# Kernel tuning notes

Measured on AMD Instinct MI355X. Metric: run time of the kernel, lower is better.

The kernel has to match this reference:

```python
import jax, jax.numpy as jnp
import numpy as np

B, H, A, D = 4096, 50, 32, 64          # batch, history len, neighbor count, embed_dim
NU, NV = 100000, 100000                # num users, num items
L = H + A                              # total gathered entries per node


def setup_inputs() -> dict:
    key = jax.random.key(0)
    ks = jax.random.split(key, 16)
    # embedding tables (u2e/v2e uniform(-1,1) as in module init, r2e ~ N(0,1) default)
    u2e = jax.random.uniform(ks[0], (NU, D), minval=-1.0, maxval=1.0, dtype=jnp.float32)
    v2e = jax.random.uniform(ks[1], (NV, D), minval=-1.0, maxval=1.0, dtype=jnp.float32)
    r2e = jax.random.normal(ks[2], (7, D), dtype=jnp.float32)
    relation_att = jax.random.normal(ks[3], (2 * D,), dtype=jnp.float32)
    s = 1.0 / np.sqrt(2 * D)  # torch Linear default init bound
    agg_W = jax.random.uniform(ks[4], (D, 2 * D), minval=-s, maxval=s, dtype=jnp.float32)
    agg_b = jax.random.uniform(ks[5], (D,), minval=-s, maxval=s, dtype=jnp.float32)
    lin1_W = jax.random.uniform(ks[6], (D, 2 * D), minval=-s, maxval=s, dtype=jnp.float32)
    lin1_b = jax.random.uniform(ks[7], (D,), minval=-s, maxval=s, dtype=jnp.float32)
    nodes_u = jax.random.randint(ks[8], (B,), 0, NU)
    nodes_v = jax.random.randint(ks[9], (B,), 0, NV)
    hist_u = jax.random.randint(ks[10], (B, H), 0, NV)   # user history = items
    hist_ur = jax.random.randint(ks[11], (B, H), 0, 6)   # ratings 0..5
    adj_u = jax.random.randint(ks[12], (B, A), 0, NU)    # social neighbors = users
    hist_v = jax.random.randint(ks[13], (B, H), 0, NU)   # item history = users
    hist_vr = jax.random.randint(ks[14], (B, H), 0, 6)
    adj_v = jax.random.randint(ks[15], (B, A), 0, NV)    # item-adj neighbors = items
    return dict(u2e=u2e, v2e=v2e, r2e=r2e, relation_att=relation_att,
                agg_W=agg_W, agg_b=agg_b, lin1_W=lin1_W, lin1_b=lin1_b,
                nodes_u=nodes_u, nodes_v=nodes_v,
                hist_u=hist_u, hist_ur=hist_ur, adj_u=adj_u,
                hist_v=hist_v, hist_vr=hist_vr, adj_v=adj_v)


def _encode(node_tab, target_tab, hist_tab, neigh_tab, r2e, relation_att,
            agg_W, agg_b, lin1_W, lin1_b, nodes, targets, hn, hr, adj):
    # Node_Encoder.forward + Node_Aggregator (percent=1.0 -> deterministic:
    # multinomial selects all indices; softmax-weighted sum is permutation-invariant).
    nf = node_tab[nodes]                                   # [B, D]
    tf = target_tab[targets]                               # [B, D]
    # query (computed as in original; with percent=1 the norm-softmax sampling
    # probability does not affect the output)
    _q = jnp.concatenate([nf, tf], axis=-1) @ agg_W.T + agg_b  # [B, D]
    hist_feat = jnp.concatenate([hist_tab[hn], neigh_tab[adj]], axis=1)  # [B, L, D]
    rates = jnp.concatenate([hr, jnp.full(adj.shape, 6, dtype=hr.dtype)], axis=1)
    rate_feat = r2e[rates]                                 # [B, L, D]
    sel = jnp.concatenate([hist_feat, rate_feat], axis=-1)  # [B, L, 2D]
    logits = jnp.einsum('ble,e->bl', sel, relation_att)    # [B, L]
    p = jax.nn.softmax(logits, axis=1)                     # softmax2 over entries
    neigh = jnp.einsum('bl,bld->bd', p, hist_feat)         # weighted sum [B, D]
    comb = jnp.concatenate([nf, neigh], axis=-1)           # [B, 2D]
    return jax.nn.relu(comb @ lin1_W.T + lin1_b)           # [B, D]


def reference(u2e, v2e, r2e, relation_att, agg_W, agg_b, lin1_W, lin1_b,
              nodes_u, nodes_v, hist_u, hist_ur, adj_u, hist_v, hist_vr, adj_v):
    # user side: isitem=False -> node=u2e, target=v2e, hist=v2e, neighbor=u2e
    eu = _encode(u2e, v2e, v2e, u2e, r2e, relation_att, agg_W, agg_b, lin1_W, lin1_b,
                 nodes_u, nodes_v, hist_u, hist_ur, adj_u)
    # item side: isitem=True -> node=v2e, target=u2e, hist=u2e, neighbor=v2e
    ev = _encode(v2e, u2e, u2e, v2e, r2e, relation_att, agg_W, agg_b, lin1_W, lin1_b,
                 nodes_v, nodes_u, hist_v, hist_vr, adj_v)
    return jnp.sum(eu * ev, axis=1)                        # [B]
```

## Files before the change

kernel.cpp:

```cpp
#include <hip/hip_runtime.h>


#define NB 4096
#define NH 50
#define NA 32
#define ND 64

__global__ void rlog_setup(const float* __restrict__ r2e,
                           const float* __restrict__ ra,
                           float* __restrict__ ws_rlog)
{
    const int lane = threadIdx.x;
    const float ra_hi = ra[64 + lane];
    #pragma unroll
    for (int r = 0; r < 7; ++r) {
        float part = r2e[r * 64 + lane] * ra_hi;
        #pragma unroll
        for (int off = 32; off >= 1; off >>= 1)
            part += __shfl_xor(part, off);
        if (lane == 0) ws_rlog[r] = part;
    }
}

__global__ __launch_bounds__(256, 8) void graphconsis_main(
    const float* __restrict__ u2e, const float* __restrict__ v2e,
    const float* __restrict__ ra,
    const float* __restrict__ lin1_W, const float* __restrict__ lin1_b,
    const int* __restrict__ nodes_u, const int* __restrict__ nodes_v,
    const int* __restrict__ hist_u, const int* __restrict__ hist_ur,
    const int* __restrict__ adj_u,
    const int* __restrict__ hist_v, const int* __restrict__ hist_vr,
    const int* __restrict__ adj_v,
    const float* __restrict__ ws_rlog,
    float* __restrict__ out)
{
    __shared__ float lds_comb[4][128];
    __shared__ float ed[4][64];

    const int wid  = threadIdx.x >> 6;
    const int lane = threadIdx.x & 63;
    const int g    = lane >> 4;
    const int j    = lane & 15;
    const int side = wid >> 1;
    const int b    = __builtin_amdgcn_readfirstlane(blockIdx.x * 2 + (wid & 1));

    const float* nodeTab  = side ? v2e : u2e;
    const float* histTab  = side ? u2e : v2e;
    const float* neighTab = side ? v2e : u2e;
    const int* nodes = side ? nodes_v : nodes_u;
    const int* hn    = side ? hist_v  : hist_u;
    const int* hr    = side ? hist_vr : hist_ur;
    const int* adj   = side ? adj_v   : adj_u;

    const float4 ra4  = *(const float4*)(ra + 4 * j);
    const float rlog6 = ws_rlog[6];

    int hidx[13];
    #pragma unroll
    for (int k = 0; k < 13; ++k) {
        int l = 4 * k + g; if (l > NH - 1) l = NH - 1;
        hidx[k] = hn[b * NH + l];
    }
    float rl0 = 0.f;
    { int l = 4 * j + g; if (l < NH) rl0 = ws_rlog[hr[b * NH + l]]; }

    float ssum = 0.f;
    float4 acc = make_float4(0.f, 0.f, 0.f, 0.f);

    #pragma unroll 4
    for (int k = 0; k < 12; ++k) {
        const float4 e = *(const float4*)(histTab + hidx[k] * ND + 4 * j);
        float part = e.x * ra4.x;
        part = fmaf(e.y, ra4.y, part);
        part = fmaf(e.z, ra4.z, part);
        part = fmaf(e.w, ra4.w, part);
        part += (j == k) ? rl0 : 0.f;
        part += __shfl_xor(part, 1);
        part += __shfl_xor(part, 2);
        part += __shfl_xor(part, 4);
        part += __shfl_xor(part, 8);
        const float p = __expf(part);
        ssum += p;
        acc.x = fmaf(p, e.x, acc.x);
        acc.y = fmaf(p, e.y, acc.y);
        acc.z = fmaf(p, e.z, acc.z);
        acc.w = fmaf(p, e.w, acc.w);
    }
    {
        const float4 e = *(const float4*)(histTab + hidx[12] * ND + 4 * j);
        float part = e.x * ra4.x;
        part = fmaf(e.y, ra4.y, part);
        part = fmaf(e.z, ra4.z, part);
        part = fmaf(e.w, ra4.w, part);
        part += (j == 12) ? rl0 : 0.f;
        part += __shfl_xor(part, 1);
        part += __shfl_xor(part, 2);
        part += __shfl_xor(part, 4);
        part += __shfl_xor(part, 8);
        const float p = (g < 2) ? __expf(part) : 0.f;
        ssum += p;
        acc.x = fmaf(p, e.x, acc.x);
        acc.y = fmaf(p, e.y, acc.y);
        acc.z = fmaf(p, e.z, acc.z);
        acc.w = fmaf(p, e.w, acc.w);
    }
    #pragma unroll 4
    for (int k = 0; k < 8; ++k) {
        const int idx = adj[b * NA + 4 * k + g];
        const float4 e = *(const float4*)(neighTab + idx * ND + 4 * j);
        float part = e.x * ra4.x;
        part = fmaf(e.y, ra4.y, part);
        part = fmaf(e.z, ra4.z, part);
        part = fmaf(e.w, ra4.w, part);
        part += __shfl_xor(part, 1);
        part += __shfl_xor(part, 2);
        part += __shfl_xor(part, 4);
        part += __shfl_xor(part, 8);
        const float p = __expf(part + rlog6);
        ssum += p;
        acc.x = fmaf(p, e.x, acc.x);
        acc.y = fmaf(p, e.y, acc.y);
        acc.z = fmaf(p, e.z, acc.z);
        acc.w = fmaf(p, e.w, acc.w);
    }

    ssum += __shfl_xor(ssum, 16);
    ssum += __shfl_xor(ssum, 32);
    acc.x += __shfl_xor(acc.x, 16); acc.x += __shfl_xor(acc.x, 32);
    acc.y += __shfl_xor(acc.y, 16); acc.y += __shfl_xor(acc.y, 32);
    acc.z += __shfl_xor(acc.z, 16); acc.z += __shfl_xor(acc.z, 32);
    acc.w += __shfl_xor(acc.w, 16); acc.w += __shfl_xor(acc.w, 32);

    const float inv = 1.0f / ssum;
    const float4 nf4 = *(const float4*)(nodeTab + nodes[b] * ND + 4 * j);

    if (g == 0) {
        *(float4*)&lds_comb[wid][4 * j] = nf4;
        float4 n4 = make_float4(acc.x * inv, acc.y * inv, acc.z * inv, acc.w * inv);
        *(float4*)&lds_comb[wid][64 + 4 * j] = n4;
    }

    float o = lin1_b[lane];
    const float4* W4 = (const float4*)(lin1_W + lane * 128);
    const float4* C4 = (const float4*)lds_comb[wid];
    #pragma unroll 8
    for (int kk = 0; kk < 32; ++kk) {
        const float4 w = W4[kk];
        const float4 c = C4[kk];
        o = fmaf(w.x, c.x, o);
        o = fmaf(w.y, c.y, o);
        o = fmaf(w.z, c.z, o);
        o = fmaf(w.w, c.w, o);
    }
    const float evec = fmaxf(o, 0.f);

    ed[wid][lane] = evec;
    __syncthreads();

    if (wid < 2) {
        float prod = ed[wid][lane] * ed[wid + 2][lane];
        #pragma unroll
        for (int off = 32; off >= 1; off >>= 1)
            prod += __shfl_xor(prod, off);
        if (lane == 0) out[blockIdx.x * 2 + wid] = prod;
    }
}

extern "C" void kernel_launch(void* const* d_in, const int* in_sizes, int n_in,
                              void* d_out, int out_size, void* d_ws, size_t ws_size,
                              hipStream_t stream)
{
    const float* u2e     = (const float*)d_in[0];
    const float* v2e     = (const float*)d_in[1];
    const float* r2e     = (const float*)d_in[2];
    const float* ra      = (const float*)d_in[3];
    const float* lin1_W  = (const float*)d_in[6];
    const float* lin1_b  = (const float*)d_in[7];
    const int* nodes_u   = (const int*)d_in[8];
    const int* nodes_v   = (const int*)d_in[9];
    const int* hist_u    = (const int*)d_in[10];
    const int* hist_ur   = (const int*)d_in[11];
    const int* adj_u     = (const int*)d_in[12];
    const int* hist_v    = (const int*)d_in[13];
    const int* hist_vr   = (const int*)d_in[14];
    const int* adj_v     = (const int*)d_in[15];
    float* out = (float*)d_out;
    float* ws_rlog = (float*)d_ws;

    hipLaunchKernelGGL(rlog_setup, dim3(1), dim3(64), 0, stream, r2e, ra, ws_rlog);
    hipLaunchKernelGGL(graphconsis_main, dim3(NB / 2), dim3(256), 0, stream,
                       u2e, v2e, ra, lin1_W, lin1_b,
                       nodes_u, nodes_v, hist_u, hist_ur, adj_u,
                       hist_v, hist_vr, adj_v, ws_rlog, out);
}
```

Before: 59.13 us.

## Fuse rating-logit setup into main kernel and prefetch all gathered rows upfront

Removes the separate single-block rlog_setup launch. Each block now computes the seven rating logits in wave 0, stores them in LDS and synchronises before use. All 21 embedding-row gathers plus the node row are issued into registers before any compute, to expose more memory-level parallelism. The launch-bounds occupancy hint is dropped, and the register arrays raise VGPR pressure, which may reduce occupancy.

```diff
diff --git a/kernel.cpp b/kernel.cpp
--- a/kernel.cpp
+++ b/kernel.cpp
@@ -6,34 +6,18 @@
 #define NA 32
 #define ND 64
 
-__global__ void rlog_setup(const float* __restrict__ r2e,
-                           const float* __restrict__ ra,
-                           float* __restrict__ ws_rlog)
-{
-    const int lane = threadIdx.x;
-    const float ra_hi = ra[64 + lane];
-    #pragma unroll
-    for (int r = 0; r < 7; ++r) {
-        float part = r2e[r * 64 + lane] * ra_hi;
-        #pragma unroll
-        for (int off = 32; off >= 1; off >>= 1)
-            part += __shfl_xor(part, off);
-        if (lane == 0) ws_rlog[r] = part;
-    }
-}
-
-__global__ __launch_bounds__(256, 8) void graphconsis_main(
+__global__ __launch_bounds__(256) void graphconsis_main(
     const float* __restrict__ u2e, const float* __restrict__ v2e,
-    const float* __restrict__ ra,
+    const float* __restrict__ r2e, const float* __restrict__ ra,
     const float* __restrict__ lin1_W, const float* __restrict__ lin1_b,
     const int* __restrict__ nodes_u, const int* __restrict__ nodes_v,
     const int* __restrict__ hist_u, const int* __restrict__ hist_ur,
     const int* __restrict__ adj_u,
     const int* __restrict__ hist_v, const int* __restrict__ hist_vr,
     const int* __restrict__ adj_v,
-    const float* __restrict__ ws_rlog,
     float* __restrict__ out)
 {
+    __shared__ float rlog_lds[8];
     __shared__ float lds_comb[4][128];
     __shared__ float ed[4][64];
 
@@ -52,8 +36,7 @@
     const int* hr    = side ? hist_vr : hist_ur;
     const int* adj   = side ? adj_v   : adj_u;
 
-    const float4 ra4  = *(const float4*)(ra + 4 * j);
-    const float rlog6 = ws_rlog[6];
+    const float4 ra4 = *(const float4*)(ra + 4 * j);
 
     int hidx[13];
     #pragma unroll
@@ -61,15 +44,46 @@
         int l = 4 * k + g; if (l > NH - 1) l = NH - 1;
         hidx[k] = hn[b * NH + l];
     }
-    float rl0 = 0.f;
-    { int l = 4 * j + g; if (l < NH) rl0 = ws_rlog[hr[b * NH + l]]; }
+    int aidx[8];
+    #pragma unroll
+    for (int k = 0; k < 8; ++k)
+        aidx[k] = adj[b * NA + 4 * k + g];
+    int hrv = 7;
+    { int l = 4 * j + g; if (l < NH) hrv = hr[b * NH + l]; }
+
+    const float4 nf4 = *(const float4*)(nodeTab + nodes[b] * ND + 4 * j);
+    float4 rh[13];
+    #pragma unroll
+    for (int k = 0; k < 13; ++k)
+        rh[k] = *(const float4*)(histTab + hidx[k] * ND + 4 * j);
+    float4 raj[8];
+    #pragma unroll
+    for (int k = 0; k < 8; ++k)
+        raj[k] = *(const float4*)(neighTab + aidx[k] * ND + 4 * j);
+
+    if (wid == 0) {
+        const float ra_hi = ra[64 + lane];
+        #pragma unroll
+        for (int r = 0; r < 7; ++r) {
+            float part = r2e[r * 64 + lane] * ra_hi;
+            #pragma unroll
+            for (int off = 32; off >= 1; off >>= 1)
+                part += __shfl_xor(part, off);
+            if (lane == 0) rlog_lds[r] = part;
+        }
+        if (lane == 0) rlog_lds[7] = 0.f;
+    }
+    __syncthreads();
+
+    const float rl0   = rlog_lds[hrv];
+    const float rlog6 = rlog_lds[6];
 
     float ssum = 0.f;
     float4 acc = make_float4(0.f, 0.f, 0.f, 0.f);
 
-    #pragma unroll 4
+    #pragma unroll
     for (int k = 0; k < 12; ++k) {
-        const float4 e = *(const float4*)(histTab + hidx[k] * ND + 4 * j);
+        const float4 e = rh[k];
         float part = e.x * ra4.x;
         part = fmaf(e.y, ra4.y, part);
         part = fmaf(e.z, ra4.z, part);
@@ -87,7 +101,7 @@
         acc.w = fmaf(p, e.w, acc.w);
     }
     {
-        const float4 e = *(const float4*)(histTab + hidx[12] * ND + 4 * j);
+        const float4 e = rh[12];
         float part = e.x * ra4.x;
         part = fmaf(e.y, ra4.y, part);
         part = fmaf(e.z, ra4.z, part);
@@ -104,10 +118,9 @@
         acc.z = fmaf(p, e.z, acc.z);
         acc.w = fmaf(p, e.w, acc.w);
     }
-    #pragma unroll 4
+    #pragma unroll
     for (int k = 0; k < 8; ++k) {
-        const int idx = adj[b * NA + 4 * k + g];
-        const float4 e = *(const float4*)(neighTab + idx * ND + 4 * j);
+        const float4 e = raj[k];
         float part = e.x * ra4.x;
         part = fmaf(e.y, ra4.y, part);
         part = fmaf(e.z, ra4.z, part);
@@ -132,7 +145,6 @@
     acc.w += __shfl_xor(acc.w, 16); acc.w += __shfl_xor(acc.w, 32);
 
     const float inv = 1.0f / ssum;
-    const float4 nf4 = *(const float4*)(nodeTab + nodes[b] * ND + 4 * j);
 
     if (g == 0) {
         *(float4*)&lds_comb[wid][4 * j] = nf4;
@@ -185,11 +197,9 @@
     const int* hist_vr   = (const int*)d_in[14];
     const int* adj_v     = (const int*)d_in[15];
     float* out = (float*)d_out;
-    float* ws_rlog = (float*)d_ws;
-
-    hipLaunchKernelGGL(rlog_setup, dim3(1), dim3(64), 0, stream, r2e, ra, ws_rlog);
+
     hipLaunchKernelGGL(graphconsis_main, dim3(NB / 2), dim3(256), 0, stream,
-                       u2e, v2e, ra, lin1_W, lin1_b,
+                       u2e, v2e, r2e, ra, lin1_W, lin1_b,
                        nodes_u, nodes_v, hist_u, hist_ur, adj_u,
-                       hist_v, hist_vr, adj_v, ws_rlog, out);
+                       hist_v, hist_vr, adj_v, out);
 }
```

New measurement: 61.48 us. +4.0%, slower.
